# Optimization experiments

Measured on AMD Instinct MI355X. Metric: run time of the kernel, lower is better.

Reference implementation:

```python
import jax, jax.numpy as jnp
import numpy as np

TOP_K = 2  # num_experts_per_tok


def setup_inputs() -> dict:
    key = jax.random.key(0)
    ks = jax.random.split(key, 4)
    B, S, H, I, E = 4, 2048, 2048, 4096, 8
    std = 0.02
    hidden_states = jax.random.normal(ks[0], (B, S, H), dtype=jnp.float32)
    gate_w = jax.random.normal(ks[1], (E, H), dtype=jnp.float32) * std   # nn.Linear weight [E,H]
    wfc = jax.random.normal(ks[2], (E, I, H), dtype=jnp.float32) * std   # c_fc weight [E,out,in]
    bfc = jnp.zeros((E, I), dtype=jnp.float32)                           # bias zero-init
    wproj = jax.random.normal(ks[3], (E, H, I), dtype=jnp.float32) * std # c_proj weight
    bproj = jnp.zeros((E, H), dtype=jnp.float32)
    return {"hidden_states": hidden_states, "gate_w": gate_w, "wfc": wfc,
            "bfc": bfc, "wproj": wproj, "bproj": bproj}


def reference(hidden_states, gate_w, wfc, bfc, wproj, bproj):
    B, S, H = hidden_states.shape
    E = wfc.shape[0]
    x = hidden_states.reshape(-1, H)                      # [T, H]
    router_logits = x @ gate_w.T                          # [T, E]
    top_vals, top_idx = jax.lax.top_k(router_logits, TOP_K)
    router_weights = jax.nn.softmax(top_vals.astype(jnp.float32), axis=-1).astype(x.dtype)  # [T, k]
    out = jnp.zeros_like(x)
    # Loop over the small fixed set of experts; each token contributes with its
    # combined gate weight for that expert (0 if not routed there). Same math as
    # the torch gather/grouped-GEMM/scatter-add path.
    for e in range(E):
        gate_e = jnp.sum(jnp.where(top_idx == e, router_weights, 0.0), axis=-1)  # [T]
        h = jax.nn.gelu(x @ wfc[e].T + bfc[e], approximate=False)                # [T, I]
        y = h @ wproj[e].T + bproj[e]                                            # [T, H]
        out = out + gate_e[:, None] * y
    return out.reshape(B, S, H), router_logits
```

## Files before the change

kernel.cpp:

```cpp
#include <hip/hip_runtime.h>
#include <hip/hip_bf16.h>
#include <math.h>

#define NT 8192
#define HD 2048
#define ID 4096
#define NE 8
#define MAXSLOT 17408
#define MAXRB 136

typedef __bf16 bf16x8 __attribute__((ext_vector_type(8)));
typedef float f32x4 __attribute__((ext_vector_type(4)));

__device__ __forceinline__ float bf2f(unsigned short u){
  union{unsigned u; float f;} v; v.u = ((unsigned)u) << 16; return v.f;
}

#define GLDS0(g, l) __builtin_amdgcn_global_load_lds( \
    (const __attribute__((address_space(1))) void*)(g), \
    (__attribute__((address_space(3))) void*)(l), 16, 0, 0)

__global__ __launch_bounds__(256) void cvt_kernel(const float* __restrict__ in,
                                                  __hip_bfloat16* __restrict__ outp, int n4){
  int i = blockIdx.x * blockDim.x + threadIdx.x;
  int stride = gridDim.x * blockDim.x;
  for (; i < n4; i += stride){
    float4 v = reinterpret_cast<const float4*>(in)[i];
    union{ushort4 u; __hip_bfloat16 h[4];} o;
    o.h[0] = __float2bfloat16(v.x); o.h[1] = __float2bfloat16(v.y);
    o.h[2] = __float2bfloat16(v.z); o.h[3] = __float2bfloat16(v.w);
    reinterpret_cast<ushort4*>(outp)[i] = o.u;
  }
}

__global__ __launch_bounds__(256) void router_kernel(
    const float* __restrict__ x, const float* __restrict__ gw,
    float* __restrict__ logits_out, int* __restrict__ tokExp,
    float* __restrict__ tokW, int* __restrict__ cnt)
{
  int wave = (blockIdx.x * blockDim.x + threadIdx.x) >> 6;
  int lane = threadIdx.x & 63;
  if (wave >= NT) return;
  const float* xr = x + (long)wave * HD;
  double acc[NE];
  #pragma unroll
  for (int e = 0; e < NE; e++) acc[e] = 0.0;
  for (int k = lane; k < HD; k += 64){
    double xv = (double)xr[k];
    #pragma unroll
    for (int e = 0; e < NE; e++) acc[e] += xv * (double)gw[e * HD + k];
  }
  #pragma unroll
  for (int e = 0; e < NE; e++){
    #pragma unroll
    for (int off = 32; off; off >>= 1) acc[e] += __shfl_down(acc[e], off, 64);
  }
  if (lane == 0){
    int e0 = 0; double v0 = acc[0];
    for (int e = 1; e < NE; e++) if (acc[e] > v0){ v0 = acc[e]; e0 = e; }
    int e1 = -1; double v1 = -1e300;
    for (int e = 0; e < NE; e++) if (e != e0 && acc[e] > v1){ v1 = acc[e]; e1 = e; }
    double ex = exp(v1 - v0);
    double s = 1.0 + ex;
    for (int e = 0; e < NE; e++) logits_out[wave * NE + e] = (float)acc[e];
    tokExp[wave * 2]     = e0; tokExp[wave * 2 + 1] = e1;
    tokW[wave * 2]       = (float)(1.0 / s);
    tokW[wave * 2 + 1]   = (float)(ex / s);
    atomicAdd(&cnt[e0], 1); atomicAdd(&cnt[e1], 1);
  }
}

__global__ void offsets_kernel(const int* __restrict__ cnt, int* __restrict__ padOff){
  if (threadIdx.x == 0 && blockIdx.x == 0){
    int o = 0;
    for (int e = 0; e < NE; e++){ padOff[e] = o; o += ((cnt[e] + 127) >> 7) << 7; }
    padOff[NE] = o;
  }
}

__global__ __launch_bounds__(256) void scatter_kernel(
    const int* __restrict__ tokExp, const float* __restrict__ tokW,
    const int* __restrict__ padOff, int* cursor,
    int* __restrict__ slotTok, int* __restrict__ tokSlot)
{
  int t = blockIdx.x * blockDim.x + threadIdx.x;
  if (t >= NT) return;
  #pragma unroll
  for (int s = 0; s < 2; s++){
    int e = tokExp[t * 2 + s];
    int pos = atomicAdd(&cursor[e], 1);
    int slot = padOff[e] + pos;
    slotTok[slot] = t;
    tokSlot[t * 2 + s] = slot;
  }
}

template<int GATHER_A, int EPI, int ND, int KD, int FUSE_CVT>
__global__ __launch_bounds__(256, 3) void moe_gemm_v12(
    const __hip_bfloat16* __restrict__ A,
    const __hip_bfloat16* __restrict__ W,
    const float* __restrict__ bias,
    const int* __restrict__ slotTok,
    const int* __restrict__ padOff,
    __hip_bfloat16* __restrict__ Yout,
    const float* __restrict__ cvIn,
    __hip_bfloat16* __restrict__ cvOut)
{
  __shared__ __align__(16) __hip_bfloat16 lds[3 * 8192];
  constexpr int NCB = ND / 128;
  constexpr int GEMM_BLKS = NCB * MAXRB;
  int cb, rb;
  if (FUSE_CVT){
    const int bid = blockIdx.x;
    if (bid >= GEMM_BLKS){
      const int n4 = NE * ID * HD / 4;
      int i = (bid - GEMM_BLKS) * 256 + (int)threadIdx.x;
      const int stride = 4096 * 256;
      for (; i < n4; i += stride){
        float4 v = reinterpret_cast<const float4*>(cvIn)[i];
        union{ushort4 u; __hip_bfloat16 h[4];} o;
        o.h[0] = __float2bfloat16(v.x); o.h[1] = __float2bfloat16(v.y);
        o.h[2] = __float2bfloat16(v.z); o.h[3] = __float2bfloat16(v.w);
        reinterpret_cast<ushort4*>(cvOut)[i] = o.u;
      }
      return;
    }
    cb = bid % NCB; rb = bid / NCB;
  } else {
    cb = blockIdx.x; rb = blockIdx.y;
  }
  if (rb * 128 >= padOff[NE]) return;
  int e = 0;
  #pragma unroll
  for (int i = 1; i < NE; i++) if (rb * 128 >= padOff[i]) e = i;

  const int tid  = threadIdx.x;
  const int lane = tid & 63;
  const int w    = tid >> 6;
  const int wr   = w >> 1, wc = w & 1;

  const int r16s = lane >> 2;
  const int cgs  = (lane & 3) ^ ((r16s >> 1) & 3);
  long aRow0, aRow1;
  {
    int g0 = rb * 128 + 32 * w + r16s, g1 = g0 + 16;
    if (GATHER_A){
      int t0 = slotTok[g0]; if (t0 < 0) t0 = 0;
      int t1 = slotTok[g1]; if (t1 < 0) t1 = 0;
      aRow0 = t0; aRow1 = t1;
    } else { aRow0 = g0; aRow1 = g1; }
  }
  const __hip_bfloat16* sA0 = A + aRow0 * (long)KD + cgs * 8;
  const __hip_bfloat16* sA1 = A + aRow1 * (long)KD + cgs * 8;
  const long bRow0 = (long)cb * 128 + 32 * w + r16s;
  const __hip_bfloat16* sB0 = W + (long)e * ND * KD + bRow0 * KD + cgs * 8;
  const __hip_bfloat16* sB1 = sB0 + 16 * (long)KD;

  __hip_bfloat16* dst0 = &lds[0 * 8192 + 2 * w * 512];
  __hip_bfloat16* dst1 = &lds[1 * 8192 + 2 * w * 512];
  __hip_bfloat16* dst2 = &lds[2 * 8192 + 2 * w * 512];

  const int r16f  = lane & 15;
  const int laneF = r16f * 32 + (((lane >> 4) ^ ((r16f >> 1) & 3))) * 8;
  const int adrA  = wr * 2048 + laneF;
  const int adrB  = 4096 + wc * 2048 + laneF;

  f32x4 acc[4][4] = {};

  constexpr int NKS = KD / 32;

#define STGADV(DP) do{ \
    GLDS0(sA0, (DP)); GLDS0(sA1, (DP) + 512); \
    GLDS0(sB0, (DP) + 4096); GLDS0(sB1, (DP) + 4096 + 512); \
    sA0 += 32; sA1 += 32; sB0 += 32; sB1 += 32; \
    asm volatile("" : "+v"(sA0), "+v"(sA1), "+v"(sB0), "+v"(sB1)); \
  }while(0)

#define RD_A(BUFC, M) (*reinterpret_cast<const bf16x8*>(&lds[(BUFC)*8192 + (M)*512 + adrA]))
#define RD_B(BUFC, N) (*reinterpret_cast<const bf16x8*>(&lds[(BUFC)*8192 + (N)*512 + adrB]))

#define BODY(K, BUFC, DP_STG) do{ \
    const int tt = t + (K); \
    if (tt < NKS){ \
      const bool dost = (tt + 2 < NKS); \
      if (dost){ STGADV(DP_STG); } \
      bf16x8 a0 = RD_A(BUFC,0), a1 = RD_A(BUFC,1), a2 = RD_A(BUFC,2), a3 = RD_A(BUFC,3); \
      bf16x8 b0 = RD_B(BUFC,0), b1 = RD_B(BUFC,1), b2 = RD_B(BUFC,2), b3 = RD_B(BUFC,3); \
      __builtin_amdgcn_s_setprio(1); \
      acc[0][0] = __builtin_amdgcn_mfma_f32_16x16x32_bf16(a0, b0, acc[0][0],0,0,0); \
      acc[1][0] = __builtin_amdgcn_mfma_f32_16x16x32_bf16(a1, b0, acc[1][0],0,0,0); \
      acc[2][0] = __builtin_amdgcn_mfma_f32_16x16x32_bf16(a2, b0, acc[2][0],0,0,0); \
      acc[3][0] = __builtin_amdgcn_mfma_f32_16x16x32_bf16(a3, b0, acc[3][0],0,0,0); \
      acc[0][1] = __builtin_amdgcn_mfma_f32_16x16x32_bf16(a0, b1, acc[0][1],0,0,0); \
      acc[1][1] = __builtin_amdgcn_mfma_f32_16x16x32_bf16(a1, b1, acc[1][1],0,0,0); \
      acc[2][1] = __builtin_amdgcn_mfma_f32_16x16x32_bf16(a2, b1, acc[2][1],0,0,0); \
      acc[3][1] = __builtin_amdgcn_mfma_f32_16x16x32_bf16(a3, b1, acc[3][1],0,0,0); \
      acc[0][2] = __builtin_amdgcn_mfma_f32_16x16x32_bf16(a0, b2, acc[0][2],0,0,0); \
      acc[1][2] = __builtin_amdgcn_mfma_f32_16x16x32_bf16(a1, b2, acc[1][2],0,0,0); \
      acc[2][2] = __builtin_amdgcn_mfma_f32_16x16x32_bf16(a2, b2, acc[2][2],0,0,0); \
      acc[3][2] = __builtin_amdgcn_mfma_f32_16x16x32_bf16(a3, b2, acc[3][2],0,0,0); \
      acc[0][3] = __builtin_amdgcn_mfma_f32_16x16x32_bf16(a0, b3, acc[0][3],0,0,0); \
      acc[1][3] = __builtin_amdgcn_mfma_f32_16x16x32_bf16(a1, b3, acc[1][3],0,0,0); \
      acc[2][3] = __builtin_amdgcn_mfma_f32_16x16x32_bf16(a2, b3, acc[2][3],0,0,0); \
      acc[3][3] = __builtin_amdgcn_mfma_f32_16x16x32_bf16(a3, b3, acc[3][3],0,0,0); \
      __builtin_amdgcn_s_setprio(0); \
      if (dost) asm volatile("s_waitcnt vmcnt(4)" ::: "memory"); \
      else      asm volatile("s_waitcnt vmcnt(0)" ::: "memory"); \
      __builtin_amdgcn_s_barrier(); \
    } \
  }while(0)

  STGADV(dst0);
  STGADV(dst1);
  asm volatile("s_waitcnt vmcnt(4)" ::: "memory");
  __builtin_amdgcn_s_barrier();

  for (int t = 0; t < NKS; t += 3){
    BODY(0, 0, dst2);
    BODY(1, 1, dst0);
    BODY(2, 2, dst1);
  }

  const int col0 = cb * 128 + wc * 64 + (lane & 15);
  const int row0 = rb * 128 + wr * 64 + (lane >> 4) * 4;
  #pragma unroll
  for (int n = 0; n < 4; n++){
    const int col = col0 + n * 16;
    const float bb = bias[(long)e * ND + col];
    #pragma unroll
    for (int m = 0; m < 4; m++){
      const long rbase = (long)(row0 + m * 16);
      #pragma unroll
      for (int r = 0; r < 4; r++){
        float v = acc[m][n][r] + bb;
        if (EPI == 0){
          float u = 0.7978845608f * (v + 0.044715f * v * v * v);
          float t2 = 1.0f - 2.0f / (__expf(2.0f * u) + 1.0f);
          v = 0.5f * v * (1.0f + t2);
        }
        Yout[(rbase + r) * ND + col] = __float2bfloat16(v);
      }
    }
  }
#undef STGADV
#undef RD_A
#undef RD_B
#undef BODY
}

__global__ __launch_bounds__(256) void combine_kernel(
    const __hip_bfloat16* __restrict__ yb,
    const int* __restrict__ tokSlot, const float* __restrict__ tokW,
    float* __restrict__ outp)
{
  const int t  = blockIdx.x;
  const int c0 = threadIdx.x * 8;
  const int s0 = tokSlot[t * 2], s1 = tokSlot[t * 2 + 1];
  const float w0 = tokW[t * 2], w1 = tokW[t * 2 + 1];
  const ushort4* p0 = reinterpret_cast<const ushort4*>(yb + (long)s0 * HD + c0);
  const ushort4* p1 = reinterpret_cast<const ushort4*>(yb + (long)s1 * HD + c0);
  float4 o[2];
  #pragma unroll
  for (int h = 0; h < 2; h++){
    ushort4 a = p0[h], b = p1[h];
    o[h].x = w0 * bf2f(a.x) + w1 * bf2f(b.x);
    o[h].y = w0 * bf2f(a.y) + w1 * bf2f(b.y);
    o[h].z = w0 * bf2f(a.z) + w1 * bf2f(b.z);
    o[h].w = w0 * bf2f(a.w) + w1 * bf2f(b.w);
  }
  float4* po = reinterpret_cast<float4*>(outp + (long)t * HD + c0);
  po[0] = o[0]; po[1] = o[1];
}

extern "C" void kernel_launch(void* const* d_in, const int* in_sizes, int n_in,
                              void* d_out, int out_size, void* d_ws, size_t ws_size,
                              hipStream_t stream)
{
  (void)in_sizes; (void)n_in; (void)out_size;
  const float* x     = (const float*)d_in[0];
  const float* gw    = (const float*)d_in[1];
  const float* wfc   = (const float*)d_in[2];
  const float* bfc   = (const float*)d_in[3];
  const float* wproj = (const float*)d_in[4];
  const float* bproj = (const float*)d_in[5];
  float* outp   = (float*)d_out;
  float* logits = outp + (size_t)NT * HD;

  char* ws = (char*)d_ws;
  size_t off = 0;
  auto alloc = [&](size_t b){ void* p = ws + off; off += (b + 255) & ~(size_t)255; return p; };

  char* shared0 = (char*)alloc((size_t)MAXSLOT * HD * 2);
  __hip_bfloat16* xb = (__hip_bfloat16*)shared0;
  __hip_bfloat16* yb = (__hip_bfloat16*)shared0;
  __hip_bfloat16* hb = (__hip_bfloat16*)alloc((size_t)MAXSLOT * ID * 2);
  int*   slotTok = (int*)alloc(MAXSLOT * 4);
  int*   tokExp  = (int*)alloc(NT * 2 * 4);
  float* tokW    = (float*)alloc(NT * 2 * 4);
  int*   tokSlot = (int*)alloc(NT * 2 * 4);
  int*   meta    = (int*)alloc(256);
  int* cnt = meta; int* cursor = meta + 8; int* padOff = meta + 16;

  const size_t WB1 = (size_t)NE * ID * HD * 2;
  const bool dual = (off + 2 * WB1) <= ws_size;
  __hip_bfloat16* wBa = (__hip_bfloat16*)(ws + off);
  __hip_bfloat16* wBb = dual ? (__hip_bfloat16*)(ws + off + WB1) : wBa;

  hipMemsetAsync(meta, 0, 256, stream);
  hipMemsetAsync(slotTok, 0xFF, MAXSLOT * 4, stream);

  cvt_kernel<<<2048, 256, 0, stream>>>(x, xb, NT * HD / 4);
  router_kernel<<<NT / 4, 256, 0, stream>>>(x, gw, logits, tokExp, tokW, cnt);
  offsets_kernel<<<1, 64, 0, stream>>>(cnt, padOff);
  scatter_kernel<<<NT / 256, 256, 0, stream>>>(tokExp, tokW, padOff, cursor, slotTok, tokSlot);

  cvt_kernel<<<4096, 256, 0, stream>>>(wfc, wBa, NE * ID * HD / 4);

  if (dual){
    moe_gemm_v12<1, 0, ID, HD, 1><<<(ID / 128) * MAXRB + 4096, 256, 0, stream>>>(
        xb, wBa, bfc, slotTok, padOff, hb, wproj, wBb);
    moe_gemm_v12<0, 1, HD, ID, 0><<<dim3(HD / 128, MAXRB), 256, 0, stream>>>(
        hb, wBb, bproj, slotTok, padOff, yb, nullptr, nullptr);
  } else {
    moe_gemm_v12<1, 0, ID, HD, 0><<<dim3(ID / 128, MAXRB), 256, 0, stream>>>(
        xb, wBa, bfc, slotTok, padOff, hb, nullptr, nullptr);
    cvt_kernel<<<4096, 256, 0, stream>>>(wproj, wBb, NE * HD * ID / 4);
    moe_gemm_v12<0, 1, HD, ID, 0><<<dim3(HD / 128, MAXRB), 256, 0, stream>>>(
        hb, wBb, bproj, slotTok, padOff, yb, nullptr, nullptr);
  }

  combine_kernel<<<NT, 256, 0, stream>>>(yb, tokSlot, tokW, outp);
}
```

Before: 1.191 ms.

## Fuse weighted combine into down-projection GEMM epilogue via atomic adds

Removes the separate combine kernel and the bf16 intermediate y buffer. The second GEMM's epilogue now multiplies each row by its routing weight and atomically adds fp32 results into the zeroed output, with slotTok encoding token*2+slot. This cuts a full write and read of the expert outputs, at the cost of an extra memset of the output and uncoalesced fp32 atomics. The results also become nondeterministic in summation order. The GELU epilogue loop is reordered so all four column values are computed per row.

```diff
diff --git a/kernel.cpp b/kernel.cpp
--- a/kernel.cpp
+++ b/kernel.cpp
@@ -79,9 +79,8 @@
 }
 
 __global__ __launch_bounds__(256) void scatter_kernel(
-    const int* __restrict__ tokExp, const float* __restrict__ tokW,
-    const int* __restrict__ padOff, int* cursor,
-    int* __restrict__ slotTok, int* __restrict__ tokSlot)
+    const int* __restrict__ tokExp, const int* __restrict__ padOff, int* cursor,
+    int* __restrict__ slotTok)
 {
   int t = blockIdx.x * blockDim.x + threadIdx.x;
   if (t >= NT) return;
@@ -89,9 +88,7 @@
   for (int s = 0; s < 2; s++){
     int e = tokExp[t * 2 + s];
     int pos = atomicAdd(&cursor[e], 1);
-    int slot = padOff[e] + pos;
-    slotTok[slot] = t;
-    tokSlot[t * 2 + s] = slot;
+    slotTok[padOff[e] + pos] = t * 2 + s;
   }
 }
 
@@ -103,6 +100,8 @@
     const int* __restrict__ slotTok,
     const int* __restrict__ padOff,
     __hip_bfloat16* __restrict__ Yout,
+    const float* __restrict__ tokWt,
+    float* __restrict__ outF,
     const float* __restrict__ cvIn,
     __hip_bfloat16* __restrict__ cvOut)
 {
@@ -145,9 +144,8 @@
   {
     int g0 = rb * 128 + 32 * w + r16s, g1 = g0 + 16;
     if (GATHER_A){
-      int t0 = slotTok[g0]; if (t0 < 0) t0 = 0;
-      int t1 = slotTok[g1]; if (t1 < 0) t1 = 0;
-      aRow0 = t0; aRow1 = t1;
+      int t0 = slotTok[g0]; aRow0 = t0 < 0 ? 0 : (t0 >> 1);
+      int t1 = slotTok[g1]; aRow1 = t1 < 0 ? 0 : (t1 >> 1);
     } else { aRow0 = g0; aRow1 = g1; }
   }
   const __hip_bfloat16* sA0 = A + aRow0 * (long)KD + cgs * 8;
@@ -223,22 +221,41 @@
 
   const int col0 = cb * 128 + wc * 64 + (lane & 15);
   const int row0 = rb * 128 + wr * 64 + (lane >> 4) * 4;
-  #pragma unroll
-  for (int n = 0; n < 4; n++){
-    const int col = col0 + n * 16;
-    const float bb = bias[(long)e * ND + col];
+  float bb[4];
+  #pragma unroll
+  for (int n = 0; n < 4; n++) bb[n] = bias[(long)e * ND + col0 + n * 16];
+
+  if (EPI == 0){
     #pragma unroll
     for (int m = 0; m < 4; m++){
       const long rbase = (long)(row0 + m * 16);
       #pragma unroll
       for (int r = 0; r < 4; r++){
-        float v = acc[m][n][r] + bb;
-        if (EPI == 0){
+        #pragma unroll
+        for (int n = 0; n < 4; n++){
+          float v = acc[m][n][r] + bb[n];
           float u = 0.7978845608f * (v + 0.044715f * v * v * v);
           float t2 = 1.0f - 2.0f / (__expf(2.0f * u) + 1.0f);
           v = 0.5f * v * (1.0f + t2);
+          Yout[rbase * ND + (long)r * ND + col0 + n * 16] = __float2bfloat16(v);
         }
-        Yout[(rbase + r) * ND + col] = __float2bfloat16(v);
+      }
+    }
+  } else {
+    #pragma unroll
+    for (int m = 0; m < 4; m++){
+      #pragma unroll
+      for (int r = 0; r < 4; r++){
+        const int pr = slotTok[row0 + m * 16 + r];
+        if (pr >= 0){
+          const long tok = pr >> 1;
+          const float wgt = tokWt[pr];
+          float* dst = outF + tok * HD + col0;
+          #pragma unroll
+          for (int n = 0; n < 4; n++){
+            atomicAdd(dst + n * 16, wgt * (acc[m][n][r] + bb[n]));
+          }
+        }
       }
     }
   }
@@ -246,30 +263,6 @@
 #undef RD_A
 #undef RD_B
 #undef BODY
-}
-
-__global__ __launch_bounds__(256) void combine_kernel(
-    const __hip_bfloat16* __restrict__ yb,
-    const int* __restrict__ tokSlot, const float* __restrict__ tokW,
-    float* __restrict__ outp)
-{
-  const int t  = blockIdx.x;
-  const int c0 = threadIdx.x * 8;
-  const int s0 = tokSlot[t * 2], s1 = tokSlot[t * 2 + 1];
-  const float w0 = tokW[t * 2], w1 = tokW[t * 2 + 1];
-  const ushort4* p0 = reinterpret_cast<const ushort4*>(yb + (long)s0 * HD + c0);
-  const ushort4* p1 = reinterpret_cast<const ushort4*>(yb + (long)s1 * HD + c0);
-  float4 o[2];
-  #pragma unroll
-  for (int h = 0; h < 2; h++){
-    ushort4 a = p0[h], b = p1[h];
-    o[h].x = w0 * bf2f(a.x) + w1 * bf2f(b.x);
-    o[h].y = w0 * bf2f(a.y) + w1 * bf2f(b.y);
-    o[h].z = w0 * bf2f(a.z) + w1 * bf2f(b.z);
-    o[h].w = w0 * bf2f(a.w) + w1 * bf2f(b.w);
-  }
-  float4* po = reinterpret_cast<float4*>(outp + (long)t * HD + c0);
-  po[0] = o[0]; po[1] = o[1];
 }
 
 extern "C" void kernel_launch(void* const* d_in, const int* in_sizes, int n_in,
@@ -290,14 +283,11 @@
   size_t off = 0;
   auto alloc = [&](size_t b){ void* p = ws + off; off += (b + 255) & ~(size_t)255; return p; };
 
-  char* shared0 = (char*)alloc((size_t)MAXSLOT * HD * 2);
-  __hip_bfloat16* xb = (__hip_bfloat16*)shared0;
-  __hip_bfloat16* yb = (__hip_bfloat16*)shared0;
+  __hip_bfloat16* xb = (__hip_bfloat16*)alloc((size_t)NT * HD * 2);
   __hip_bfloat16* hb = (__hip_bfloat16*)alloc((size_t)MAXSLOT * ID * 2);
   int*   slotTok = (int*)alloc(MAXSLOT * 4);
   int*   tokExp  = (int*)alloc(NT * 2 * 4);
   float* tokW    = (float*)alloc(NT * 2 * 4);
-  int*   tokSlot = (int*)alloc(NT * 2 * 4);
   int*   meta    = (int*)alloc(256);
   int* cnt = meta; int* cursor = meta + 8; int* padOff = meta + 16;
 
@@ -308,26 +298,25 @@
 
   hipMemsetAsync(meta, 0, 256, stream);
   hipMemsetAsync(slotTok, 0xFF, MAXSLOT * 4, stream);
+  hipMemsetAsync(outp, 0, (size_t)NT * HD * 4, stream);
 
   cvt_kernel<<<2048, 256, 0, stream>>>(x, xb, NT * HD / 4);
   router_kernel<<<NT / 4, 256, 0, stream>>>(x, gw, logits, tokExp, tokW, cnt);
   offsets_kernel<<<1, 64, 0, stream>>>(cnt, padOff);
-  scatter_kernel<<<NT / 256, 256, 0, stream>>>(tokExp, tokW, padOff, cursor, slotTok, tokSlot);
+  scatter_kernel<<<NT / 256, 256, 0, stream>>>(tokExp, padOff, cursor, slotTok);
 
   cvt_kernel<<<4096, 256, 0, stream>>>(wfc, wBa, NE * ID * HD / 4);
 
   if (dual){
     moe_gemm_v12<1, 0, ID, HD, 1><<<(ID / 128) * MAXRB + 4096, 256, 0, stream>>>(
-        xb, wBa, bfc, slotTok, padOff, hb, wproj, wBb);
+        xb, wBa, bfc, slotTok, padOff, hb, nullptr, nullptr, wproj, wBb);
     moe_gemm_v12<0, 1, HD, ID, 0><<<dim3(HD / 128, MAXRB), 256, 0, stream>>>(
-        hb, wBb, bproj, slotTok, padOff, yb, nullptr, nullptr);
+        hb, wBb, bproj, slotTok, padOff, nullptr, tokW, outp, nullptr, nullptr);
   } else {
     moe_gemm_v12<1, 0, ID, HD, 0><<<dim3(ID / 128, MAXRB), 256, 0, stream>>>(
-        xb, wBa, bfc, slotTok, padOff, hb, nullptr, nullptr);
+        xb, wBa, bfc, slotTok, padOff, hb, nullptr, nullptr, nullptr, nullptr);
     cvt_kernel<<<4096, 256, 0, stream>>>(wproj, wBb, NE * HD * ID / 4);
     moe_gemm_v12<0, 1, HD, ID, 0><<<dim3(HD / 128, MAXRB), 256, 0, stream>>>(
-        hb, wBb, bproj, slotTok, padOff, yb, nullptr, nullptr);
-  }
-
-  combine_kernel<<<NT, 256, 0, stream>>>(yb, tokSlot, tokW, outp);
-}
+        hb, wBb, bproj, slotTok, padOff, nullptr, tokW, outp, nullptr, nullptr);
+  }
+}
```

After: 1.209 ms. Within noise of the previous version (+1.5%).
